# Performance work log

Measured on AMD Instinct MI355X. Metric: run time of the kernel, lower is better.

The kernel has to match this reference:

```python
import jax, jax.numpy as jnp
import numpy as np

EPS = 1e-12  # torch F.normalize eps


def setup_inputs() -> dict:
    key = jax.random.key(0)
    k1, k2, k3, k4, k5 = jax.random.split(key, 5)
    n_drug1 = n_drug2 = 4096
    d = 128
    n_pairs = 1_000_000
    association_pairs = jax.random.randint(k1, (2, n_pairs), 0, n_drug1, dtype=jnp.int64) if jax.config.jax_enable_x64 else jax.random.randint(k1, (2, n_pairs), 0, n_drug1, dtype=jnp.int32)
    drug_embedding1 = jax.random.normal(k2, (n_drug1, d), dtype=jnp.float32)
    drug_embedding2 = jax.random.normal(k3, (n_drug2, d), dtype=jnp.float32)
    W1 = jax.random.normal(k4, (d, n_drug1), dtype=jnp.float32) * (1.0 / np.sqrt(n_drug1))
    W2 = jax.random.normal(k5, (d, n_drug2), dtype=jnp.float32) * (1.0 / np.sqrt(n_drug2))
    return {
        "association_pairs": association_pairs,
        "drug_embedding1": drug_embedding1,
        "drug_embedding2": drug_embedding2,
        "W1": W1,
        "W2": W2,
    }


def reference(association_pairs, drug_embedding1, drug_embedding2, W1, W2):
    # Original does Linear(diag(ones)) which is mathematically W.T; the
    # projected "embedding table" for drug i is column i of W.
    # Gather: table1[idx] == W1[:, idx].T -> [n_pairs, d]
    e1 = jnp.take(W1, association_pairs[0], axis=1).T  # [P, d]
    e2 = jnp.take(W2, association_pairs[1], axis=1).T  # [P, d]
    assoc = e1 * e2                                     # [P, d]
    # F.normalize: x / max(||x||_2, eps) along dim=1
    norm = jnp.linalg.norm(assoc, axis=1, keepdims=True)
    assoc = assoc / jnp.maximum(norm, EPS)
    # dropout in eval mode -> identity
    return assoc
```

## Files before the change

kernel.cpp:

```cpp
#include <hip/hip_runtime.h>
#include <hip/hip_bf16.h>


#define D 128

using f32x4 = __attribute__((ext_vector_type(4))) float;
using u16x4 = __attribute__((ext_vector_type(4))) unsigned short;

__device__ __forceinline__ float bf2f(unsigned short u) {
    return __uint_as_float(((unsigned int)u) << 16);
}

__global__ __launch_bounds__(256) void transpose_tables(
        const float* __restrict__ W1, const float* __restrict__ W2,
        __hip_bfloat16* __restrict__ T1, __hip_bfloat16* __restrict__ T2,
        int n_drug) {
    __shared__ float tile[32][33];
    const float*    W = blockIdx.z ? W2 : W1;
    __hip_bfloat16* T = blockIdx.z ? T2 : T1;
    int jt = blockIdx.x * 32;
    int kt = blockIdx.y * 32;
    int tx = threadIdx.x;
    int ty = threadIdx.y;
    #pragma unroll
    for (int r = ty; r < 32; r += 8)
        tile[r][tx] = W[(size_t)(kt + r) * n_drug + jt + tx];
    __syncthreads();
    #pragma unroll
    for (int r = ty; r < 32; r += 8)
        T[(size_t)(jt + r) * D + kt + tx] = __float2bfloat16(tile[tx][r]);
}

#define LOAD_ROW(dst0, dst1, dst2, dst3, idx0, idx1)                          \
    {                                                                         \
        const u16x4* base1 =                                                  \
            reinterpret_cast<const u16x4*>(T1 + (size_t)(idx0)*D);            \
        const u16x4* base2 =                                                  \
            reinterpret_cast<const u16x4*>(T2 + (size_t)(idx1)*D);            \
        dst0 = base1[lane];                                                   \
        dst1 = base1[lane + 16];                                              \
        dst2 = base2[lane];                                                   \
        dst3 = base2[lane + 16];                                              \
    }

__global__ __launch_bounds__(256) void gather_mul_normalize(
        const int* __restrict__ pairs,
        const __hip_bfloat16* __restrict__ T1,
        const __hip_bfloat16* __restrict__ T2,
        float* __restrict__ out,
        int n_pairs, int n_groups) {
    const int lane  = threadIdx.x & 15;
    const int group = blockIdx.x * (blockDim.x >> 4) + (threadIdx.x >> 4);
    if (group >= n_pairs) return;
    const int last = n_pairs - 1;

    int row = group;
    int i0 = pairs[row];
    int i1 = pairs[n_pairs + row];
    u16x4 a0, a1, b0, b1;
    LOAD_ROW(a0, a1, b0, b1, i0, i1);

    int r1 = row + n_groups;
    int r1c = r1 <= last ? r1 : last;
    int j0 = pairs[r1c];
    int j1 = pairs[n_pairs + r1c];
    u16x4 c0, c1, d0, d1;
    LOAD_ROW(c0, c1, d0, d1, j0, j1);

    int r2 = r1 + n_groups;
    int r2c = r2 <= last ? r2 : last;
    int k0 = pairs[r2c];
    int k1 = pairs[n_pairs + r2c];

    for (;;) {
        u16x4 e0, e1, f0, f1;
        LOAD_ROW(e0, e1, f0, f1, k0, k1);

        int r3  = r2 + n_groups;
        int r3c = r3 <= last ? r3 : last;
        int l0 = pairs[r3c];
        int l1 = pairs[n_pairs + r3c];

        float p[8];
        #pragma unroll
        for (int q = 0; q < 4; ++q) {
            p[q]     = bf2f(a0[q]) * bf2f(b0[q]);
            p[q + 4] = bf2f(a1[q]) * bf2f(b1[q]);
        }
        float s = 0.f;
        #pragma unroll
        for (int q = 0; q < 8; ++q) s += p[q] * p[q];
        #pragma unroll
        for (int m = 8; m >= 1; m >>= 1) s += __shfl_xor(s, m);
        float inv = 1.0f / fmaxf(sqrtf(s), 1e-12f);
        f32x4 q0 = {p[0] * inv, p[1] * inv, p[2] * inv, p[3] * inv};
        f32x4 q1 = {p[4] * inv, p[5] * inv, p[6] * inv, p[7] * inv};
        f32x4* orow = reinterpret_cast<f32x4*>(out + (size_t)row * D);
        __builtin_nontemporal_store(q0, orow + lane);
        __builtin_nontemporal_store(q1, orow + lane + 16);

        if (r1 > last) break;
        row = r1;
        a0 = c0; a1 = c1; b0 = d0; b1 = d1;
        c0 = e0; c1 = e1; d0 = f0; d1 = f1;
        r1 = r2; r2 = r3;
        k0 = l0; k1 = l1;
    }
}

extern "C" void kernel_launch(void* const* d_in, const int* in_sizes, int n_in,
                              void* d_out, int out_size, void* d_ws, size_t ws_size,
                              hipStream_t stream) {
    const int*   pairs = (const int*)d_in[0];
    const float* W1    = (const float*)d_in[3];
    const float* W2    = (const float*)d_in[4];
    float*       out   = (float*)d_out;

    int n_pairs = in_sizes[0] / 2;
    int n_drug  = in_sizes[3] / D;

    __hip_bfloat16* T1 = (__hip_bfloat16*)d_ws;
    __hip_bfloat16* T2 = T1 + (size_t)n_drug * D;

    {
        dim3 grid(n_drug / 32, D / 32, 2);
        dim3 block(32, 8, 1);
        transpose_tables<<<grid, block, 0, stream>>>(W1, W2, T1, T2, n_drug);
    }
    {
        int blocks   = 2048;
        int n_groups = blocks * (256 / 16);
        gather_mul_normalize<<<blocks, 256, 0, stream>>>(pairs, T1, T2, out,
                                                         n_pairs, n_groups);
    }
}
```

Measured before the change: 108.3 us.

## Deepen gather software pipeline to two rows per stage and use rsq

Restructures the grid-stride gather loop so each 16-lane group keeps two rows in flight per stage, with ping-pong buffers (E/O) and index prefetch four to five strides ahead. This doubles the outstanding memory loads per thread to hide gather latency. It also replaces the sqrt-and-divide with a clamped v_rsq_f32 via inline asm. The cost is more registers per thread and slightly different rounding in the normalization.

Result: no change. 109.1 us (+0.7%).

```diff
diff --git a/kernel.cpp b/kernel.cpp
--- a/kernel.cpp
+++ b/kernel.cpp
@@ -31,80 +31,92 @@
         T[(size_t)(jt + r) * D + kt + tx] = __float2bfloat16(tile[tx][r]);
 }
 
-#define LOAD_ROW(dst0, dst1, dst2, dst3, idx0, idx1)                          \
-    {                                                                         \
-        const u16x4* base1 =                                                  \
-            reinterpret_cast<const u16x4*>(T1 + (size_t)(idx0)*D);            \
-        const u16x4* base2 =                                                  \
-            reinterpret_cast<const u16x4*>(T2 + (size_t)(idx1)*D);            \
-        dst0 = base1[lane];                                                   \
-        dst1 = base1[lane + 16];                                              \
-        dst2 = base2[lane];                                                   \
-        dst3 = base2[lane + 16];                                              \
+struct Row { u16x4 a0, a1, b0, b1; };
+
+__device__ __forceinline__ Row load_row(const __hip_bfloat16* T1,
+                                        const __hip_bfloat16* T2,
+                                        int i0, int i1, int lane) {
+    Row r;
+    const u16x4* p1 = reinterpret_cast<const u16x4*>(T1 + (size_t)i0 * D);
+    const u16x4* p2 = reinterpret_cast<const u16x4*>(T2 + (size_t)i1 * D);
+    r.a0 = p1[lane];
+    r.a1 = p1[lane + 16];
+    r.b0 = p2[lane];
+    r.b1 = p2[lane + 16];
+    return r;
+}
+
+__device__ __forceinline__ void compute_store(const Row& r, int row, bool ok,
+                                              float* __restrict__ out,
+                                              int lane) {
+    float p[8];
+    #pragma unroll
+    for (int q = 0; q < 4; ++q) {
+        p[q]     = bf2f(r.a0[q]) * bf2f(r.b0[q]);
+        p[q + 4] = bf2f(r.a1[q]) * bf2f(r.b1[q]);
     }
+    float s = 0.f;
+    #pragma unroll
+    for (int q = 0; q < 8; ++q) s += p[q] * p[q];
+    #pragma unroll
+    for (int m = 8; m >= 1; m >>= 1) s += __shfl_xor(s, m);
+    s = fmaxf(s, 1e-24f);
+    float inv;
+    asm("v_rsq_f32 %0, %1" : "=v"(inv) : "v"(s));
+    if (ok) {
+        f32x4 q0 = {p[0] * inv, p[1] * inv, p[2] * inv, p[3] * inv};
+        f32x4 q1 = {p[4] * inv, p[5] * inv, p[6] * inv, p[7] * inv};
+        f32x4* orow = reinterpret_cast<f32x4*>(out + (size_t)row * D);
+        __builtin_nontemporal_store(q0, orow + lane);
+        __builtin_nontemporal_store(q1, orow + lane + 16);
+    }
+}
 
 __global__ __launch_bounds__(256) void gather_mul_normalize(
         const int* __restrict__ pairs,
         const __hip_bfloat16* __restrict__ T1,
         const __hip_bfloat16* __restrict__ T2,
         float* __restrict__ out,
-        int n_pairs, int n_groups) {
+        int n_pairs, int S) {
     const int lane  = threadIdx.x & 15;
     const int group = blockIdx.x * (blockDim.x >> 4) + (threadIdx.x >> 4);
     if (group >= n_pairs) return;
     const int last = n_pairs - 1;
 
-    int row = group;
-    int i0 = pairs[row];
-    int i1 = pairs[n_pairs + row];
-    u16x4 a0, a1, b0, b1;
-    LOAD_ROW(a0, a1, b0, b1, i0, i1);
+    int ra = group;
+    int t;
 
-    int r1 = row + n_groups;
-    int r1c = r1 <= last ? r1 : last;
-    int j0 = pairs[r1c];
-    int j1 = pairs[n_pairs + r1c];
-    u16x4 c0, c1, d0, d1;
-    LOAD_ROW(c0, c1, d0, d1, j0, j1);
+    t = ra + S; t = t <= last ? t : last;
+    Row E0 = load_row(T1, T2, pairs[ra], pairs[n_pairs + ra], lane);
+    Row E1 = load_row(T1, T2, pairs[t],  pairs[n_pairs + t],  lane);
 
-    int r2 = r1 + n_groups;
-    int r2c = r2 <= last ? r2 : last;
-    int k0 = pairs[r2c];
-    int k1 = pairs[n_pairs + r2c];
+    t = ra + 2 * S; t = t <= last ? t : last;
+    int ja0 = pairs[t], ja1 = pairs[n_pairs + t];
+    t = ra + 3 * S; t = t <= last ? t : last;
+    int jb0 = pairs[t], jb1 = pairs[n_pairs + t];
 
+    int ia0, ia1, ib0, ib1;
     for (;;) {
-        u16x4 e0, e1, f0, f1;
-        LOAD_ROW(e0, e1, f0, f1, k0, k1);
+        Row O0 = load_row(T1, T2, ja0, ja1, lane);
+        Row O1 = load_row(T1, T2, jb0, jb1, lane);
+        t = ra + 4 * S; t = t <= last ? t : last;
+        ia0 = pairs[t]; ia1 = pairs[n_pairs + t];
+        t = ra + 5 * S; t = t <= last ? t : last;
+        ib0 = pairs[t]; ib1 = pairs[n_pairs + t];
+        compute_store(E0, ra,     true,            out, lane);
+        compute_store(E1, ra + S, ra + S <= last,  out, lane);
+        if (ra + 2 * S > last) break;
 
-        int r3  = r2 + n_groups;
-        int r3c = r3 <= last ? r3 : last;
-        int l0 = pairs[r3c];
-        int l1 = pairs[n_pairs + r3c];
-
-        float p[8];
-        #pragma unroll
-        for (int q = 0; q < 4; ++q) {
-            p[q]     = bf2f(a0[q]) * bf2f(b0[q]);
-            p[q + 4] = bf2f(a1[q]) * bf2f(b1[q]);
-        }
-        float s = 0.f;
-        #pragma unroll
-        for (int q = 0; q < 8; ++q) s += p[q] * p[q];
-        #pragma unroll
-        for (int m = 8; m >= 1; m >>= 1) s += __shfl_xor(s, m);
-        float inv = 1.0f / fmaxf(sqrtf(s), 1e-12f);
-        f32x4 q0 = {p[0] * inv, p[1] * inv, p[2] * inv, p[3] * inv};
-        f32x4 q1 = {p[4] * inv, p[5] * inv, p[6] * inv, p[7] * inv};
-        f32x4* orow = reinterpret_cast<f32x4*>(out + (size_t)row * D);
-        __builtin_nontemporal_store(q0, orow + lane);
-        __builtin_nontemporal_store(q1, orow + lane + 16);
-
-        if (r1 > last) break;
-        row = r1;
-        a0 = c0; a1 = c1; b0 = d0; b1 = d1;
-        c0 = e0; c1 = e1; d0 = f0; d1 = f1;
-        r1 = r2; r2 = r3;
-        k0 = l0; k1 = l1;
+        E0 = load_row(T1, T2, ia0, ia1, lane);
+        E1 = load_row(T1, T2, ib0, ib1, lane);
+        t = ra + 6 * S; t = t <= last ? t : last;
+        ja0 = pairs[t]; ja1 = pairs[n_pairs + t];
+        t = ra + 7 * S; t = t <= last ? t : last;
+        jb0 = pairs[t]; jb1 = pairs[n_pairs + t];
+        compute_store(O0, ra + 2 * S, true,                out, lane);
+        compute_store(O1, ra + 3 * S, ra + 3 * S <= last,  out, lane);
+        ra += 4 * S;
+        if (ra > last) break;
     }
 }
 
@@ -128,9 +140,9 @@
         transpose_tables<<<grid, block, 0, stream>>>(W1, W2, T1, T2, n_drug);
     }
     {
-        int blocks   = 2048;
-        int n_groups = blocks * (256 / 16);
+        int blocks = 2048;
+        int S      = blocks * (256 / 16);
         gather_mul_normalize<<<blocks, 256, 0, stream>>>(pairs, T1, T2, out,
-                                                         n_pairs, n_groups);
+                                                         n_pairs, S);
     }
 }
```
